# Optimization experiments

Measured on AMD Instinct MI355X. Metric: run time of the kernel, lower is better.

The kernel has to match this reference:

```python
import jax, jax.numpy as jnp
import numpy as np

EMBED_DIM = 768
HEADS = 8
HEAD_DIM = 128  # gnn_hidden_dim
OUT_DIM = HEADS * HEAD_DIM  # 1024, concat=True
NEG_SLOPE = 0.2  # PyG GATConv leaky_relu slope


def setup_inputs() -> dict:
    key = jax.random.key(0)
    ks = jax.random.split(key, 12)
    N, E = 10000, 160000
    x = jax.random.normal(ks[0], (N, EMBED_DIM), dtype=jnp.float32)
    edge_index = jax.random.randint(ks[1], (2, E), 0, N, dtype=jnp.int32)
    edge_attr = jax.random.uniform(ks[2], (E, 1), dtype=jnp.float32)
    # GATConv params (single layer, edge_dim=1)
    sc = 1.0 / np.sqrt(EMBED_DIM)
    W = jax.random.normal(ks[3], (EMBED_DIM, OUT_DIM), dtype=jnp.float32) * sc
    att_src = jax.random.normal(ks[4], (HEADS, HEAD_DIM), dtype=jnp.float32) * 0.1
    att_dst = jax.random.normal(ks[5], (HEADS, HEAD_DIM), dtype=jnp.float32) * 0.1
    W_edge = jax.random.normal(ks[6], (1, OUT_DIM), dtype=jnp.float32)
    att_edge = jax.random.normal(ks[7], (HEADS, HEAD_DIM), dtype=jnp.float32) * 0.1
    bias = jnp.zeros((OUT_DIM,), dtype=jnp.float32)
    # final classifier: in = 3*OUT_DIM (global pool + text node + image node)
    clf_W = jax.random.normal(ks[8], (3 * OUT_DIM, 2), dtype=jnp.float32) * (1.0 / np.sqrt(3 * OUT_DIM))
    clf_b = jnp.zeros((2,), dtype=jnp.float32)
    return {
        'x': x, 'edge_index': edge_index, 'edge_attr': edge_attr,
        'text_idx': 0, 'image_idx': 1,
        'W': W, 'att_src': att_src, 'att_dst': att_dst,
        'W_edge': W_edge, 'att_edge': att_edge, 'bias': bias,
        'clf_W': clf_W, 'clf_b': clf_b,
    }


def gat_layer(x, edge_index, edge_attr, W, att_src, att_dst, W_edge, att_edge, bias):
    N = x.shape[0]
    # add self-loops with edge_attr = mean of existing edge_attr (PyG default fill_value='mean')
    loop = jnp.arange(N, dtype=edge_index.dtype)
    ei = jnp.concatenate([edge_index, jnp.stack([loop, loop])], axis=1)
    ea_mean = jnp.mean(edge_attr, axis=0, keepdims=True)
    ea = jnp.concatenate([edge_attr, jnp.broadcast_to(ea_mean, (N, edge_attr.shape[1]))], axis=0)
    src, dst = ei[0], ei[1]
    xs = (x @ W).reshape(N, HEADS, HEAD_DIM)             # [N, H, C]
    a_src = jnp.einsum('nhc,hc->nh', xs, att_src)        # per-node src logits
    a_dst = jnp.einsum('nhc,hc->nh', xs, att_dst)
    e_emb = (ea @ W_edge).reshape(-1, HEADS, HEAD_DIM)   # [Etot, H, C]
    a_edge = jnp.einsum('ehc,hc->eh', e_emb, att_edge)
    alpha = jax.nn.leaky_relu(a_src[src] + a_dst[dst] + a_edge, NEG_SLOPE)  # [Etot, H]
    # softmax over incoming edges of each dst node
    m = jax.ops.segment_max(alpha, dst, num_segments=N)
    ex = jnp.exp(alpha - m[dst])
    denom = jax.ops.segment_sum(ex, dst, num_segments=N)
    w = ex / denom[dst]                                  # normalized attention [Etot, H]
    msg = xs[src] * w[:, :, None]                        # [Etot, H, C]
    out = jax.ops.segment_sum(msg, dst, num_segments=N)  # [N, H, C]
    return out.reshape(N, OUT_DIM) + bias


def reference(x, edge_index, edge_attr, text_idx, image_idx,
              W, att_src, att_dst, W_edge, att_edge, bias, clf_W, clf_b):
    # single GAT layer (num_gat_layers=1 -> no ELU/dropout after, eval mode)
    h = gat_layer(x, edge_index, edge_attr, W, att_src, att_dst, W_edge, att_edge, bias)
    g = jnp.mean(h, axis=0, keepdims=True)               # global_mean_pool, batch=None
    t = h[text_idx][None, :]
    im = h[image_idx][None, :]
    fused = jnp.concatenate([g, t, im], axis=1)          # [1, 3*OUT_DIM]
    logits = fused @ clf_W + clf_b                       # [1, 2]
    return logits
```

## Files before the change

kernel.cpp:

```cpp
#include <hip/hip_runtime.h>

#define NN 10000
#define EE 160000
#define ETOT (EE + NN)
#define EMB 768
#define ODIM 1024
#define NEG 0.2f
#define CAP 56

#define OFF_P      0
#define OFF_Q      12288
#define OFF_EAACC  12296
#define OFF_CNTD   12304
#define OFF_CNTS   22304
#define ZERO_START 12296
#define ZERO_CNT   20008
#define OFF_A      32304
#define OFF_APART  192304
#define OFF_SRCD   1472304
#define OFF_DSTS   2032304
#define OFF_PACK   2592304
#define OFF_EXD    2762304
#define OFF_EXS    7242304
#define OFF_RDEN   11722304
#define OFF_S      11802304
#define OFF_Z      11882304
#define OFF_YPART  11894592
#define OFF_FPART  12859200

__global__ __launch_bounds__(256) void k1f(
    const float* __restrict__ W, const float* __restrict__ att_src,
    const float* __restrict__ att_dst, const float* __restrict__ W_edge,
    const float* __restrict__ att_edge, const float* __restrict__ edge_attr,
    const int* __restrict__ ei, float* __restrict__ ws) {
  int b = blockIdx.x;
  if (b < 48) {
    int tid = b * 256 + threadIdx.x;
    int k = tid >> 4, j = tid & 15, h = j & 7;
    const float* att = (j < 8) ? att_src : att_dst;
    const float* wp = W + k * ODIM + h * 128;
    const float* ap = att + h * 128;
    float acc = 0.f;
    #pragma unroll 8
    for (int c = 0; c < 128; ++c) acc += wp[c] * ap[c];
    ws[OFF_P + k * 16 + j] = acc;
  } else if (b == 48) {
    if (threadIdx.x < 8) {
      int h = threadIdx.x;
      float acc = 0.f;
      #pragma unroll 8
      for (int c = 0; c < 128; ++c) acc += W_edge[h * 128 + c] * att_edge[h * 128 + c];
      ws[OFF_Q + h] = acc;
    }
  } else if (b < 113) {
    int bi = b - 49;
    float acc = 0.f;
    for (int i = bi * 256 + threadIdx.x; i < EE; i += 64 * 256) acc += edge_attr[i];
    #pragma unroll
    for (int off = 32; off > 0; off >>= 1) acc += __shfl_down(acc, off, 64);
    if ((threadIdx.x & 63) == 0) atomicAdd(&ws[OFF_EAACC], acc);
  } else {
    int e = (b - 113) * 256 + threadIdx.x;
    if (e >= ETOT) return;
    int src, dst;
    if (e < EE) { src = ei[e]; dst = ei[EE + e]; } else { src = dst = e - EE; }
    int* cntd = (int*)(ws + OFF_CNTD);
    int* cnts = (int*)(ws + OFF_CNTS);
    int pd = atomicAdd(&cntd[dst], 1);
    if (pd < CAP) ((int*)(ws + OFF_SRCD))[dst * CAP + pd] = src;
    int ps = atomicAdd(&cnts[src], 1);
    if (ps < CAP) ((int*)(ws + OFF_DSTS))[src * CAP + ps] = dst;
    ((int*)(ws + OFF_PACK))[e] = (pd & 0xffff) | (ps << 16);
  }
}

__global__ __launch_bounds__(256) void k3_part(const float* __restrict__ x,
                                               float* __restrict__ ws) {
  __shared__ float pL[96 * 16];
  const int c = blockIdx.y;
  const int kbase = c * 96;
  for (int i = threadIdx.x; i < 96 * 16; i += 256) pL[i] = ws[OFF_P + kbase * 16 + i];
  __syncthreads();
  int n = blockIdx.x * 256 + threadIdx.x;
  if (n >= NN) return;
  float acc[16];
  #pragma unroll
  for (int j = 0; j < 16; ++j) acc[j] = 0.f;
  const float4* xr = (const float4*)(x + n * EMB + kbase);
  for (int kk = 0; kk < 24; ++kk) {
    float4 xv = xr[kk];
    const float* pr = &pL[kk * 64];
    #pragma unroll
    for (int j = 0; j < 16; ++j) acc[j] += xv.x * pr[j];
    #pragma unroll
    for (int j = 0; j < 16; ++j) acc[j] += xv.y * pr[16 + j];
    #pragma unroll
    for (int j = 0; j < 16; ++j) acc[j] += xv.z * pr[32 + j];
    #pragma unroll
    for (int j = 0; j < 16; ++j) acc[j] += xv.w * pr[48 + j];
  }
  float4* ap = (float4*)(ws + OFF_APART + c * 160000 + n * 16);
  ap[0] = make_float4(acc[0], acc[1], acc[2], acc[3]);
  ap[1] = make_float4(acc[4], acc[5], acc[6], acc[7]);
  ap[2] = make_float4(acc[8], acc[9], acc[10], acc[11]);
  ap[3] = make_float4(acc[12], acc[13], acc[14], acc[15]);
}

__global__ __launch_bounds__(256) void k_reduceA(float* __restrict__ ws) {
  int i = blockIdx.x * 256 + threadIdx.x;
  if (i >= 40000) return;
  float4 r = make_float4(0.f, 0.f, 0.f, 0.f);
  #pragma unroll
  for (int c = 0; c < 8; ++c) {
    float4 a = ((const float4*)(ws + OFF_APART + c * 160000))[i];
    r.x += a.x; r.y += a.y; r.z += a.z; r.w += a.w;
  }
  ((float4*)(ws + OFF_A))[i] = r;
}

__global__ __launch_bounds__(256) void kE(const int* __restrict__ ei,
                                          const float* __restrict__ edge_attr,
                                          float* __restrict__ ws) {
  int e = blockIdx.x * 256 + threadIdx.x;
  if (e >= ETOT) return;
  int src, dst; float ea;
  if (e < EE) { src = ei[e]; dst = ei[EE + e]; ea = edge_attr[e]; }
  else { src = dst = e - EE; ea = ws[OFF_EAACC] * (1.0f / EE); }
  int pk = ((const int*)(ws + OFF_PACK))[e];
  int pd = pk & 0xffff, ps = pk >> 16;
  const float4* as4 = (const float4*)(ws + OFF_A + src * 16);
  const float4* ad4 = (const float4*)(ws + OFF_A + dst * 16 + 8);
  float4 s0 = as4[0], s1 = as4[1], d0 = ad4[0], d1 = ad4[1];
  float asrc[8] = {s0.x, s0.y, s0.z, s0.w, s1.x, s1.y, s1.z, s1.w};
  float adst[8] = {d0.x, d0.y, d0.z, d0.w, d1.x, d1.y, d1.z, d1.w};
  float ex[8];
  #pragma unroll
  for (int h = 0; h < 8; ++h) {
    float v = asrc[h] + adst[h] + ea * ws[OFF_Q + h];
    v = (v >= 0.f) ? v : NEG * v;
    ex[h] = __expf(v);
  }
  float4 e0 = make_float4(ex[0], ex[1], ex[2], ex[3]);
  float4 e1 = make_float4(ex[4], ex[5], ex[6], ex[7]);
  if (pd < CAP) {
    float4* p = (float4*)(ws + OFF_EXD + (dst * CAP + pd) * 8);
    p[0] = e0; p[1] = e1;
  }
  if (ps < CAP) {
    float4* p = (float4*)(ws + OFF_EXS + (src * CAP + ps) * 8);
    p[0] = e0; p[1] = e1;
  }
}

__global__ __launch_bounds__(256) void kD(float* __restrict__ ws) {
  int t = blockIdx.x * 256 + threadIdx.x;
  if (t >= NN * 8) return;
  int dst = t >> 3, h = t & 7;
  int deg = ((const int*)(ws + OFF_CNTD))[dst];
  if (deg > CAP) deg = CAP;
  const float* base = ws + OFF_EXD + dst * (CAP * 8) + h;
  float den = 0.f;
  for (int j = 0; j < deg; ++j) den += base[j * 8];
  ws[OFF_RDEN + dst * 8 + h] = 1.0f / den;
}

__global__ __launch_bounds__(256) void kSZ(const float* __restrict__ x,
                                           const int* __restrict__ tptr,
                                           const int* __restrict__ iptr,
                                           float* __restrict__ ws) {
  if (blockIdx.x < 313) {
    int t = blockIdx.x * 256 + threadIdx.x;
    if (t >= NN * 8) return;
    int src = t >> 3, h = t & 7;
    int deg = ((const int*)(ws + OFF_CNTS))[src];
    if (deg > CAP) deg = CAP;
    const int* dstrow = (const int*)(ws + OFF_DSTS) + src * CAP;
    const float* exrow = ws + OFF_EXS + src * (CAP * 8) + h;
    float s = 0.f;
    for (int j = 0; j < deg; ++j)
      s += exrow[j * 8] * ws[OFF_RDEN + dstrow[j] * 8 + h];
    ws[OFF_S + src * 8 + h] = s;
  } else {
    __shared__ float wL[CAP * 8];
    __shared__ int srcS[CAP];
    __shared__ int degS;
    int r = blockIdx.x - 313;
    int d = r / 3, ky = r % 3;
    int target = (d == 0) ? tptr[0] : iptr[0];
    if (threadIdx.x == 0) {
      int dg = ((const int*)(ws + OFF_CNTD))[target];
      degS = (dg > CAP) ? CAP : dg;
    }
    __syncthreads();
    int deg = degS;
    for (int idx = threadIdx.x; idx < deg * 8; idx += 256) {
      int j = idx >> 3, h = idx & 7;
      wL[idx] = ws[OFF_EXD + (target * CAP + j) * 8 + h]
              * ws[OFF_RDEN + target * 8 + h];
      if (h == 0) srcS[j] = ((const int*)(ws + OFF_SRCD))[target * CAP + j];
    }
    __syncthreads();
    int col = ky * 256 + threadIdx.x;
    float acc[8];
    #pragma unroll
    for (int h = 0; h < 8; ++h) acc[h] = 0.f;
    for (int j = 0; j < deg; ++j) {
      float xv = x[srcS[j] * EMB + col];
      const float* wv = &wL[j * 8];
      #pragma unroll
      for (int h = 0; h < 8; ++h) acc[h] += wv[h] * xv;
    }
    #pragma unroll
    for (int h = 0; h < 8; ++h) ws[OFF_Z + (d * 8 + h) * EMB + col] = acc[h];
  }
}

__global__ __launch_bounds__(256) void k7s(const float* __restrict__ x,
                                           float* __restrict__ ws) {
  __shared__ float sL[64 * 8];
  int base = blockIdx.x * 64;
  int c = blockIdx.y;
  for (int i = threadIdx.x; i < 512; i += 256) {
    int n = base + (i >> 3);
    sL[i] = (n < NN) ? ws[OFF_S + base * 8 + i] : 0.f;
  }
  __syncthreads();
  int col = c * 256 + threadIdx.x;
  float acc[8];
  #pragma unroll
  for (int h = 0; h < 8; ++h) acc[h] = 0.f;
  int nmax = (NN - base < 64) ? (NN - base) : 64;
  for (int i = 0; i < nmax; ++i) {
    float xv = x[(base + i) * EMB + col];
    const float* sv = &sL[i * 8];
    #pragma unroll
    for (int h = 0; h < 8; ++h) acc[h] += xv * sv[h];
  }
  float* yp = ws + OFF_YPART + (blockIdx.x * 3 + c) * 2048;
  #pragma unroll
  for (int h = 0; h < 8; ++h) yp[h * 256 + threadIdx.x] = acc[h];
}

__global__ __launch_bounds__(128) void k8_part(const float* __restrict__ W,
                                               float* __restrict__ ws) {
  __shared__ float vL[3 * 96];
  int h = blockIdx.x, kc = blockIdx.y;
  int kbase = kc * 96;
  for (int k = threadIdx.x; k < 96; k += 128) {
    int col = kbase + k, cc = col >> 8, ck = col & 255;
    float acc = 0.f;
    for (int b = 0; b < 157; ++b)
      acc += ws[OFF_YPART + (b * 3 + cc) * 2048 + h * 256 + ck];
    vL[k] = acc * (1.0f / NN);
  }
  for (int i = threadIdx.x; i < 192; i += 128) {
    int d = i / 96, k = i - d * 96;
    vL[96 + i] = ws[OFF_Z + (d * 8 + h) * EMB + kbase + k];
  }
  __syncthreads();
  int c = threadIdx.x;
  float a0 = 0.f, a1 = 0.f, a2 = 0.f;
  #pragma unroll 4
  for (int k = 0; k < 96; ++k) {
    float wv = W[(kbase + k) * ODIM + h * 128 + c];
    a0 += vL[k] * wv;
    a1 += vL[96 + k] * wv;
    a2 += vL[192 + k] * wv;
  }
  float* fp = ws + OFF_FPART + kc * 3072 + h * 128 + c;
  fp[0] = a0; fp[1024] = a1; fp[2048] = a2;
}

__global__ __launch_bounds__(256) void k9_logits(const float* __restrict__ clf_W,
                                                 const float* __restrict__ clf_b,
                                                 const float* __restrict__ bias,
                                                 const float* __restrict__ ws,
                                                 float* __restrict__ out) {
  float a0 = 0.f, a1 = 0.f;
  for (int i = threadIdx.x; i < 3072; i += 256) {
    float f = bias[i & 1023];
    #pragma unroll
    for (int kc = 0; kc < 8; ++kc) f += ws[OFF_FPART + kc * 3072 + i];
    a0 += f * clf_W[i * 2 + 0];
    a1 += f * clf_W[i * 2 + 1];
  }
  #pragma unroll
  for (int off = 32; off > 0; off >>= 1) {
    a0 += __shfl_down(a0, off, 64);
    a1 += __shfl_down(a1, off, 64);
  }
  __shared__ float r0[4], r1[4];
  int wid = threadIdx.x >> 6, lane = threadIdx.x & 63;
  if (lane == 0) { r0[wid] = a0; r1[wid] = a1; }
  __syncthreads();
  if (threadIdx.x == 0) {
    out[0] = r0[0] + r0[1] + r0[2] + r0[3] + clf_b[0];
    out[1] = r1[0] + r1[1] + r1[2] + r1[3] + clf_b[1];
  }
}

extern "C" void kernel_launch(void* const* d_in, const int* in_sizes, int n_in,
                              void* d_out, int out_size, void* d_ws, size_t ws_size,
                              hipStream_t stream) {
  const float* x        = (const float*)d_in[0];
  const int*   ei       = (const int*)d_in[1];
  const float* edge_attr= (const float*)d_in[2];
  const int*   tptr     = (const int*)d_in[3];
  const int*   iptr     = (const int*)d_in[4];
  const float* W        = (const float*)d_in[5];
  const float* att_src  = (const float*)d_in[6];
  const float* att_dst  = (const float*)d_in[7];
  const float* W_edge   = (const float*)d_in[8];
  const float* att_edge = (const float*)d_in[9];
  const float* bias     = (const float*)d_in[10];
  const float* clf_W    = (const float*)d_in[11];
  const float* clf_b    = (const float*)d_in[12];
  float* ws  = (float*)d_ws;
  float* out = (float*)d_out;

  hipMemsetAsync(ws + ZERO_START, 0, ZERO_CNT * sizeof(float), stream);
  k1f<<<778, 256, 0, stream>>>(W, att_src, att_dst, W_edge, att_edge, edge_attr, ei, ws);
  dim3 g3(40, 8);
  k3_part<<<g3, 256, 0, stream>>>(x, ws);
  k_reduceA<<<157, 256, 0, stream>>>(ws);
  kE<<<665, 256, 0, stream>>>(ei, edge_attr, ws);
  kD<<<313, 256, 0, stream>>>(ws);
  kSZ<<<319, 256, 0, stream>>>(x, tptr, iptr, ws);
  dim3 g7(157, 3);
  k7s<<<g7, 256, 0, stream>>>(x, ws);
  dim3 g8(8, 8);
  k8_part<<<g8, 128, 0, stream>>>(W, ws);
  k9_logits<<<1, 256, 0, stream>>>(clf_W, clf_b, bias, ws, out);
}
```

Baseline: 200.2 us.

## Fuse GAT pipeline into one cooperative persistent kernel with grid syncs

Replaces the memset plus ten-kernel chain with a single cooperative kernel that runs each stage as a grid-strided work loop separated by grid.sync(). The attention-logit projection now does the full K reduction per node, which removes the partial buffer and its separate reduce pass. Node sums are fused with the x-weighted column sums, and the final projection writes logits directly with atomics onto a bias-initialised output. The aim is to remove launch gaps and intermediate traffic, at the cost of grid-sync overhead and a grid capped at 512 blocks. The old multi-kernel path stays as a fallback when cooperative launch is unavailable.

```diff
diff --git a/kernel.cpp b/kernel.cpp
--- a/kernel.cpp
+++ b/kernel.cpp
@@ -1,4 +1,7 @@
 #include <hip/hip_runtime.h>
+#include <hip/hip_cooperative_groups.h>
+
+namespace cg = cooperative_groups;
 
 #define NN 10000
 #define EE 160000
@@ -7,28 +10,331 @@
 #define ODIM 1024
 #define NEG 0.2f
 #define CAP 56
+#define TPB 256
 
 #define OFF_P      0
 #define OFF_Q      12288
-#define OFF_EAACC  12296
-#define OFF_CNTD   12304
-#define OFF_CNTS   22304
-#define ZERO_START 12296
-#define ZERO_CNT   20008
-#define OFF_A      32304
-#define OFF_APART  192304
-#define OFF_SRCD   1472304
-#define OFF_DSTS   2032304
-#define OFF_PACK   2592304
-#define OFF_EXD    2762304
-#define OFF_EXS    7242304
-#define OFF_RDEN   11722304
-#define OFF_S      11802304
-#define OFF_Z      11882304
-#define OFF_YPART  11894592
-#define OFF_FPART  12859200
-
-__global__ __launch_bounds__(256) void k1f(
+#define OFF_EAP    12296
+#define OFF_EAACC  12552
+#define OFF_CNTD   12556
+#define OFF_CNTS   22556
+#define OFF_A      32556
+#define OFF_SRCD   192556
+#define OFF_DSTS   752556
+#define OFF_PACK   1312556
+#define OFF_EXD    1482556
+#define OFF_EXS    5962556
+#define OFF_RDEN   10442556
+#define OFF_Z      10522556
+#define OFF_YPART  10534844
+
+__global__ __launch_bounds__(TPB, 2) void mega(
+    const float* __restrict__ x, const int* __restrict__ ei,
+    const float* __restrict__ edge_attr, const int* __restrict__ tptr,
+    const int* __restrict__ iptr, const float* __restrict__ W,
+    const float* __restrict__ att_src, const float* __restrict__ att_dst,
+    const float* __restrict__ W_edge, const float* __restrict__ att_edge,
+    const float* __restrict__ bias, const float* __restrict__ clf_W,
+    const float* __restrict__ clf_b, float* __restrict__ ws,
+    float* __restrict__ out) {
+  __shared__ float smem[6144];
+  cg::grid_group grid = cg::this_grid();
+  const int t = threadIdx.x, bid = blockIdx.x;
+  const int GS = gridDim.x;
+  int* wsI = (int*)ws;
+
+  for (int i = bid * TPB + t; i < 20000; i += GS * TPB) wsI[OFF_CNTD + i] = 0;
+  for (int u = bid; u < 113; u += GS) {
+    if (u < 48) {
+      int tid = u * TPB + t, k = tid >> 4, j = tid & 15, h = j & 7;
+      const float* att = (j < 8) ? att_src : att_dst;
+      const float* wp = W + k * ODIM + h * 128;
+      const float* ap = att + h * 128;
+      float acc = 0.f;
+      #pragma unroll 8
+      for (int c = 0; c < 128; ++c) acc += wp[c] * ap[c];
+      ws[OFF_P + k * 16 + j] = acc;
+    } else if (u == 48) {
+      if (t < 8) {
+        float acc = 0.f;
+        #pragma unroll 8
+        for (int c = 0; c < 128; ++c) acc += W_edge[t * 128 + c] * att_edge[t * 128 + c];
+        ws[OFF_Q + t] = acc;
+      }
+    } else {
+      int ue = u - 49;
+      float acc = 0.f;
+      for (int i = ue * TPB + t; i < EE; i += 64 * TPB) acc += edge_attr[i];
+      #pragma unroll
+      for (int o = 32; o > 0; o >>= 1) acc += __shfl_down(acc, o, 64);
+      if ((t & 63) == 0) ws[OFF_EAP + ue * 4 + (t >> 6)] = acc;
+    }
+  }
+  grid.sync();
+
+  for (int u = bid; u < 980; u += GS) {
+    if (u < 313) {
+      int n = u * 32 + (t & 31);
+      int jp = (t >> 5) * 2;
+      float a0 = 0.f, a1 = 0.f;
+      const float4* xr = (const float4*)(x + n * EMB);
+      for (int half = 0; half < 2; ++half) {
+        __syncthreads();
+        for (int i = t; i < 1536; i += TPB)
+          ((float4*)smem)[i] = ((const float4*)(ws + OFF_P + half * 6144))[i];
+        __syncthreads();
+        if (n < NN) {
+          for (int kk = 0; kk < 96; ++kk) {
+            float4 xv = xr[half * 96 + kk];
+            int k4 = kk * 64 + jp;
+            float2 p0 = *(const float2*)&smem[k4];
+            float2 p1 = *(const float2*)&smem[k4 + 16];
+            float2 p2 = *(const float2*)&smem[k4 + 32];
+            float2 p3 = *(const float2*)&smem[k4 + 48];
+            a0 += xv.x * p0.x + xv.y * p1.x + xv.z * p2.x + xv.w * p3.x;
+            a1 += xv.x * p0.y + xv.y * p1.y + xv.z * p2.y + xv.w * p3.y;
+          }
+        }
+      }
+      if (n < NN) {
+        ws[OFF_A + n * 16 + jp] = a0;
+        ws[OFF_A + n * 16 + jp + 1] = a1;
+      }
+    } else if (u < 978) {
+      int e = (u - 313) * TPB + t;
+      if (e < ETOT) {
+        int src, dst;
+        if (e < EE) { src = ei[e]; dst = ei[EE + e]; } else { src = dst = e - EE; }
+        int pd = atomicAdd(&wsI[OFF_CNTD + dst], 1);
+        if (pd < CAP) wsI[OFF_SRCD + dst * CAP + pd] = src;
+        int ps = atomicAdd(&wsI[OFF_CNTS + src], 1);
+        if (ps < CAP) wsI[OFF_DSTS + src * CAP + ps] = dst;
+        if (pd > CAP) pd = CAP;
+        if (ps > CAP) ps = CAP;
+        wsI[OFF_PACK + e] = pd | (ps << 16);
+      }
+    } else if (u == 978) {
+      float a = 0.f;
+      if (t < 64)
+        a = ws[OFF_EAP + t] + ws[OFF_EAP + t + 64] + ws[OFF_EAP + t + 128]
+          + ws[OFF_EAP + t + 192];
+      #pragma unroll
+      for (int o = 32; o > 0; o >>= 1) a += __shfl_down(a, o, 64);
+      if (t == 0) ws[OFF_EAACC] = a;
+    }
+  }
+  grid.sync();
+
+  for (int u = bid; u < 666; u += GS) {
+    if (u < 665) {
+      int e = u * TPB + t;
+      if (e < ETOT) {
+        int src, dst; float ea;
+        if (e < EE) { src = ei[e]; dst = ei[EE + e]; ea = edge_attr[e]; }
+        else { src = dst = e - EE; ea = ws[OFF_EAACC] * (1.0f / EE); }
+        int pk = wsI[OFF_PACK + e];
+        int pd = pk & 0xffff, ps = pk >> 16;
+        const float4* as4 = (const float4*)(ws + OFF_A + src * 16);
+        const float4* ad4 = (const float4*)(ws + OFF_A + dst * 16 + 8);
+        float4 s0 = as4[0], s1 = as4[1], d0 = ad4[0], d1 = ad4[1];
+        float asr[8] = {s0.x, s0.y, s0.z, s0.w, s1.x, s1.y, s1.z, s1.w};
+        float ads[8] = {d0.x, d0.y, d0.z, d0.w, d1.x, d1.y, d1.z, d1.w};
+        float ex[8];
+        #pragma unroll
+        for (int h = 0; h < 8; ++h) {
+          float v = asr[h] + ads[h] + ea * ws[OFF_Q + h];
+          v = (v >= 0.f) ? v : NEG * v;
+          ex[h] = __expf(v);
+        }
+        float4 e0 = make_float4(ex[0], ex[1], ex[2], ex[3]);
+        float4 e1 = make_float4(ex[4], ex[5], ex[6], ex[7]);
+        if (pd < CAP) {
+          float4* p = (float4*)(ws + OFF_EXD + (dst * CAP + pd) * 8);
+          p[0] = e0; p[1] = e1;
+        }
+        if (ps < CAP) {
+          float4* p = (float4*)(ws + OFF_EXS + (src * CAP + ps) * 8);
+          p[0] = e0; p[1] = e1;
+        }
+      }
+    } else {
+      float b0 = 0.f, b1 = 0.f;
+      for (int i = t; i < 3072; i += TPB) {
+        float f = bias[i & 1023];
+        b0 += f * clf_W[2 * i];
+        b1 += f * clf_W[2 * i + 1];
+      }
+      #pragma unroll
+      for (int o = 32; o > 0; o >>= 1) {
+        b0 += __shfl_down(b0, o, 64);
+        b1 += __shfl_down(b1, o, 64);
+      }
+      __syncthreads();
+      if ((t & 63) == 0) { smem[t >> 6] = b0; smem[4 + (t >> 6)] = b1; }
+      __syncthreads();
+      if (t == 0) {
+        out[0] = clf_b[0] + smem[0] + smem[1] + smem[2] + smem[3];
+        out[1] = clf_b[1] + smem[4] + smem[5] + smem[6] + smem[7];
+      }
+    }
+  }
+  grid.sync();
+
+  for (int u = bid; u < 313; u += GS) {
+    int tg = u * TPB + t;
+    if (tg < 80000) {
+      int dst = tg >> 3, h = tg & 7;
+      int deg = wsI[OFF_CNTD + dst]; if (deg > CAP) deg = CAP;
+      const float* bp = ws + OFF_EXD + dst * (CAP * 8) + h;
+      float den = 0.f;
+      for (int j = 0; j < deg; ++j) den += bp[j * 8];
+      ws[OFF_RDEN + tg] = 1.0f / den;
+    }
+  }
+  grid.sync();
+
+  for (int u = bid; u < 163; u += GS) {
+    if (u < 157) {
+      int base = u * 64;
+      for (int w = t; w < 512; w += TPB) {
+        int n = base + (w >> 3), h = w & 7;
+        float s = 0.f;
+        if (n < NN) {
+          int deg = wsI[OFF_CNTS + n]; if (deg > CAP) deg = CAP;
+          const float* er = ws + OFF_EXS + n * (CAP * 8) + h;
+          const int* dr = wsI + OFF_DSTS + n * CAP;
+          for (int j = 0; j < deg; ++j)
+            s += er[j * 8] * ws[OFF_RDEN + dr[j] * 8 + h];
+        }
+        smem[w] = s;
+      }
+      __syncthreads();
+      int nmax = NN - base; if (nmax > 64) nmax = 64;
+      float acc[24];
+      #pragma unroll
+      for (int q = 0; q < 24; ++q) acc[q] = 0.f;
+      for (int i = 0; i < nmax; ++i) {
+        const float* xr = x + (base + i) * EMB;
+        float x0 = xr[t], x1 = xr[t + 256], x2 = xr[t + 512];
+        const float* sv = &smem[i * 8];
+        #pragma unroll
+        for (int h = 0; h < 8; ++h) {
+          acc[h] += x0 * sv[h];
+          acc[8 + h] += x1 * sv[h];
+          acc[16 + h] += x2 * sv[h];
+        }
+      }
+      float* yp = ws + OFF_YPART + u * 6144;
+      #pragma unroll
+      for (int h = 0; h < 8; ++h) {
+        yp[h * 768 + t] = acc[h];
+        yp[h * 768 + 256 + t] = acc[8 + h];
+        yp[h * 768 + 512 + t] = acc[16 + h];
+      }
+      __syncthreads();
+    } else {
+      int r = u - 157, d = r / 3, ky = r % 3;
+      int target = (d == 0) ? tptr[0] : iptr[0];
+      float* wL = smem;
+      int* srcS = (int*)(smem + 448);
+      int* degP = (int*)(smem + 508);
+      if (t == 0) { int dg = wsI[OFF_CNTD + target]; degP[0] = (dg > CAP) ? CAP : dg; }
+      __syncthreads();
+      int deg = degP[0];
+      for (int idx = t; idx < deg * 8; idx += TPB) {
+        int j = idx >> 3, h = idx & 7;
+        wL[idx] = ws[OFF_EXD + (target * CAP + j) * 8 + h] * ws[OFF_RDEN + target * 8 + h];
+        if (h == 0) srcS[j] = wsI[OFF_SRCD + target * CAP + j];
+      }
+      __syncthreads();
+      int col = ky * 256 + t;
+      float acc[8];
+      #pragma unroll
+      for (int h = 0; h < 8; ++h) acc[h] = 0.f;
+      for (int j = 0; j < deg; ++j) {
+        float xv = x[srcS[j] * EMB + col];
+        const float* wv = &wL[j * 8];
+        #pragma unroll
+        for (int h = 0; h < 8; ++h) acc[h] += wv[h] * xv;
+      }
+      #pragma unroll
+      for (int h = 0; h < 8; ++h) ws[OFF_Z + (d * 8 + h) * EMB + col] = acc[h];
+      __syncthreads();
+    }
+  }
+  grid.sync();
+
+  for (int u = bid; u < 64; u += GS) {
+    int h = u >> 3, kc = u & 7, kbase = kc * 96;
+    float* vY2 = smem;
+    float* vL  = smem + 192;
+    if (t < 192) {
+      int k = t % 96, half = t / 96;
+      float a = 0.f;
+      for (int b = half; b < 157; b += 2)
+        a += ws[OFF_YPART + b * 6144 + h * 768 + kbase + k];
+      vY2[t] = a;
+    } else {
+      for (int i = t - 192; i < 192; i += 64) {
+        int d = i / 96, k = i - d * 96;
+        vL[96 + i] = ws[OFF_Z + (d * 8 + h) * EMB + kbase + k];
+      }
+    }
+    __syncthreads();
+    if (t < 96) vL[t] = (vY2[t] + vY2[t + 96]) * (1.0f / NN);
+    __syncthreads();
+    float l0 = 0.f, l1 = 0.f;
+    if (t < 128) {
+      int c = t;
+      float a0 = 0.f, a1 = 0.f, a2 = 0.f;
+      #pragma unroll 4
+      for (int k = 0; k < 96; ++k) {
+        float wv = W[(kbase + k) * ODIM + h * 128 + c];
+        a0 += vL[k] * wv;
+        a1 += vL[96 + k] * wv;
+        a2 += vL[192 + k] * wv;
+      }
+      int ib = h * 128 + c;
+      l0 = a0 * clf_W[2 * ib] + a1 * clf_W[2 * (1024 + ib)] + a2 * clf_W[2 * (2048 + ib)];
+      l1 = a0 * clf_W[2 * ib + 1] + a1 * clf_W[2 * (1024 + ib) + 1] + a2 * clf_W[2 * (2048 + ib) + 1];
+    }
+    #pragma unroll
+    for (int o = 32; o > 0; o >>= 1) {
+      l0 += __shfl_down(l0, o, 64);
+      l1 += __shfl_down(l1, o, 64);
+    }
+    __syncthreads();
+    if ((t & 63) == 0) { smem[480 + (t >> 6)] = l0; smem[484 + (t >> 6)] = l1; }
+    __syncthreads();
+    if (t == 0) {
+      atomicAdd(&out[0], smem[480] + smem[481] + smem[482] + smem[483]);
+      atomicAdd(&out[1], smem[484] + smem[485] + smem[486] + smem[487]);
+    }
+    __syncthreads();
+  }
+}
+
+#define FB_P      0
+#define FB_Q      12288
+#define FB_EAACC  12296
+#define FB_CNTD   12304
+#define FB_CNTS   22304
+#define FB_ZSTART 12296
+#define FB_ZCNT   20008
+#define FB_A      32304
+#define FB_APART  192304
+#define FB_SRCD   1472304
+#define FB_DSTS   2032304
+#define FB_PACK   2592304
+#define FB_EXD    2762304
+#define FB_EXS    7242304
+#define FB_RDEN   11722304
+#define FB_S      11802304
+#define FB_Z      11882304
+#define FB_YPART  11894592
+#define FB_FPART  12859200
+
+__global__ __launch_bounds__(256) void f_k1f(
     const float* __restrict__ W, const float* __restrict__ att_src,
     const float* __restrict__ att_dst, const float* __restrict__ W_edge,
     const float* __restrict__ att_edge, const float* __restrict__ edge_attr,
@@ -43,14 +349,14 @@
     float acc = 0.f;
     #pragma unroll 8
     for (int c = 0; c < 128; ++c) acc += wp[c] * ap[c];
-    ws[OFF_P + k * 16 + j] = acc;
+    ws[FB_P + k * 16 + j] = acc;
   } else if (b == 48) {
     if (threadIdx.x < 8) {
       int h = threadIdx.x;
       float acc = 0.f;
       #pragma unroll 8
       for (int c = 0; c < 128; ++c) acc += W_edge[h * 128 + c] * att_edge[h * 128 + c];
-      ws[OFF_Q + h] = acc;
+      ws[FB_Q + h] = acc;
     }
   } else if (b < 113) {
     int bi = b - 49;
@@ -58,28 +364,30 @@
     for (int i = bi * 256 + threadIdx.x; i < EE; i += 64 * 256) acc += edge_attr[i];
     #pragma unroll
     for (int off = 32; off > 0; off >>= 1) acc += __shfl_down(acc, off, 64);
-    if ((threadIdx.x & 63) == 0) atomicAdd(&ws[OFF_EAACC], acc);
+    if ((threadIdx.x & 63) == 0) atomicAdd(&ws[FB_EAACC], acc);
   } else {
     int e = (b - 113) * 256 + threadIdx.x;
     if (e >= ETOT) return;
     int src, dst;
     if (e < EE) { src = ei[e]; dst = ei[EE + e]; } else { src = dst = e - EE; }
-    int* cntd = (int*)(ws + OFF_CNTD);
-    int* cnts = (int*)(ws + OFF_CNTS);
+    int* cntd = (int*)(ws + FB_CNTD);
+    int* cnts = (int*)(ws + FB_CNTS);
     int pd = atomicAdd(&cntd[dst], 1);
-    if (pd < CAP) ((int*)(ws + OFF_SRCD))[dst * CAP + pd] = src;
+    if (pd < CAP) ((int*)(ws + FB_SRCD))[dst * CAP + pd] = src;
     int ps = atomicAdd(&cnts[src], 1);
-    if (ps < CAP) ((int*)(ws + OFF_DSTS))[src * CAP + ps] = dst;
-    ((int*)(ws + OFF_PACK))[e] = (pd & 0xffff) | (ps << 16);
-  }
-}
-
-__global__ __launch_bounds__(256) void k3_part(const float* __restrict__ x,
-                                               float* __restrict__ ws) {
+    if (ps < CAP) ((int*)(ws + FB_DSTS))[src * CAP + ps] = dst;
+    if (pd > CAP) pd = CAP;
+    if (ps > CAP) ps = CAP;
+    ((int*)(ws + FB_PACK))[e] = pd | (ps << 16);
+  }
+}
+
+__global__ __launch_bounds__(256) void f_k3part(const float* __restrict__ x,
+                                                float* __restrict__ ws) {
   __shared__ float pL[96 * 16];
   const int c = blockIdx.y;
   const int kbase = c * 96;
-  for (int i = threadIdx.x; i < 96 * 16; i += 256) pL[i] = ws[OFF_P + kbase * 16 + i];
+  for (int i = threadIdx.x; i < 96 * 16; i += 256) pL[i] = ws[FB_P + kbase * 16 + i];
   __syncthreads();
   int n = blockIdx.x * 256 + threadIdx.x;
   if (n >= NN) return;
@@ -99,87 +407,87 @@
     #pragma unroll
     for (int j = 0; j < 16; ++j) acc[j] += xv.w * pr[48 + j];
   }
-  float4* ap = (float4*)(ws + OFF_APART + c * 160000 + n * 16);
+  float4* ap = (float4*)(ws + FB_APART + c * 160000 + n * 16);
   ap[0] = make_float4(acc[0], acc[1], acc[2], acc[3]);
   ap[1] = make_float4(acc[4], acc[5], acc[6], acc[7]);
   ap[2] = make_float4(acc[8], acc[9], acc[10], acc[11]);
   ap[3] = make_float4(acc[12], acc[13], acc[14], acc[15]);
 }
 
-__global__ __launch_bounds__(256) void k_reduceA(float* __restrict__ ws) {
+__global__ __launch_bounds__(256) void f_reduceA(float* __restrict__ ws) {
   int i = blockIdx.x * 256 + threadIdx.x;
   if (i >= 40000) return;
   float4 r = make_float4(0.f, 0.f, 0.f, 0.f);
   #pragma unroll
   for (int c = 0; c < 8; ++c) {
-    float4 a = ((const float4*)(ws + OFF_APART + c * 160000))[i];
+    float4 a = ((const float4*)(ws + FB_APART + c * 160000))[i];
     r.x += a.x; r.y += a.y; r.z += a.z; r.w += a.w;
   }
-  ((float4*)(ws + OFF_A))[i] = r;
-}
-
-__global__ __launch_bounds__(256) void kE(const int* __restrict__ ei,
-                                          const float* __restrict__ edge_attr,
-                                          float* __restrict__ ws) {
+  ((float4*)(ws + FB_A))[i] = r;
+}
+
+__global__ __launch_bounds__(256) void f_kE(const int* __restrict__ ei,
+                                            const float* __restrict__ edge_attr,
+                                            float* __restrict__ ws) {
   int e = blockIdx.x * 256 + threadIdx.x;
   if (e >= ETOT) return;
   int src, dst; float ea;
   if (e < EE) { src = ei[e]; dst = ei[EE + e]; ea = edge_attr[e]; }
-  else { src = dst = e - EE; ea = ws[OFF_EAACC] * (1.0f / EE); }
-  int pk = ((const int*)(ws + OFF_PACK))[e];
+  else { src = dst = e - EE; ea = ws[FB_EAACC] * (1.0f / EE); }
+  int pk = ((const int*)(ws + FB_PACK))[e];
   int pd = pk & 0xffff, ps = pk >> 16;
-  const float4* as4 = (const float4*)(ws + OFF_A + src * 16);
-  const float4* ad4 = (const float4*)(ws + OFF_A + dst * 16 + 8);
+  const float4* as4 = (const float4*)(ws + FB_A + src * 16);
+  const float4* ad4 = (const float4*)(ws + FB_A + dst * 16 + 8);
   float4 s0 = as4[0], s1 = as4[1], d0 = ad4[0], d1 = ad4[1];
-  float asrc[8] = {s0.x, s0.y, s0.z, s0.w, s1.x, s1.y, s1.z, s1.w};
-  float adst[8] = {d0.x, d0.y, d0.z, d0.w, d1.x, d1.y, d1.z, d1.w};
+  float asr[8] = {s0.x, s0.y, s0.z, s0.w, s1.x, s1.y, s1.z, s1.w};
+  float ads[8] = {d0.x, d0.y, d0.z, d0.w, d1.x, d1.y, d1.z, d1.w};
   float ex[8];
   #pragma unroll
   for (int h = 0; h < 8; ++h) {
-    float v = asrc[h] + adst[h] + ea * ws[OFF_Q + h];
+    float v = asr[h] + ads[h] + ea * ws[FB_Q + h];
     v = (v >= 0.f) ? v : NEG * v;
     ex[h] = __expf(v);
   }
   float4 e0 = make_float4(ex[0], ex[1], ex[2], ex[3]);
   float4 e1 = make_float4(ex[4], ex[5], ex[6], ex[7]);
   if (pd < CAP) {
-    float4* p = (float4*)(ws + OFF_EXD + (dst * CAP + pd) * 8);
+    float4* p = (float4*)(ws + FB_EXD + (dst * CAP + pd) * 8);
     p[0] = e0; p[1] = e1;
   }
   if (ps < CAP) {
-    float4* p = (float4*)(ws + OFF_EXS + (src * CAP + ps) * 8);
+    float4* p = (float4*)(ws + FB_EXS + (src * CAP + ps) * 8);
     p[0] = e0; p[1] = e1;
   }
 }
 
-__global__ __launch_bounds__(256) void kD(float* __restrict__ ws) {
+__global__ __launch_bounds__(256) void f_kD(float* __restrict__ ws) {
   int t = blockIdx.x * 256 + threadIdx.x;
   if (t >= NN * 8) return;
   int dst = t >> 3, h = t & 7;
-  int deg = ((const int*)(ws + OFF_CNTD))[dst];
+  int deg = ((const int*)(ws + FB_CNTD))[dst];
   if (deg > CAP) deg = CAP;
-  const float* base = ws + OFF_EXD + dst * (CAP * 8) + h;
+  const float* base = ws + FB_EXD + dst * (CAP * 8) + h;
   float den = 0.f;
   for (int j = 0; j < deg; ++j) den += base[j * 8];
-  ws[OFF_RDEN + dst * 8 + h] = 1.0f / den;
-}
-
-__global__ __launch_bounds__(256) void kSZ(const float* __restrict__ x,
-                                           const int* __restrict__ tptr,
-                                           const int* __restrict__ iptr,
-                                           float* __restrict__ ws) {
+  ws[FB_RDEN + dst * 8 + h] = 1.0f / den;
+}
+
+__global__ __launch_bounds__(256) void f_kSZ(const float* __restrict__ x,
+                                             const int* __restrict__ tptr,
+                                             const int* __restrict__ iptr,
+                                             float* __restrict__ ws) {
   if (blockIdx.x < 313) {
     int t = blockIdx.x * 256 + threadIdx.x;
     if (t >= NN * 8) return;
     int src = t >> 3, h = t & 7;
-    int deg = ((const int*)(ws + OFF_CNTS))[src];
+    int deg = ((const int*)(ws + FB_CNTS))[src];
     if (deg > CAP) deg = CAP;
-    const int* dstrow = (const int*)(ws + OFF_DSTS) + src * CAP;
-    const float* exrow = ws + OFF_EXS + src * (CAP * 8) + h;
+    const int* dstrow = (const int*)(ws + FB_DSTS) + src * CAP;
+    const float* exrow = ws + FB_EXS + src * (CAP * 8) + h;
     float s = 0.f;
     for (int j = 0; j < deg; ++j)
-      s += exrow[j * 8] * ws[OFF_RDEN + dstrow[j] * 8 + h];
-    ws[OFF_S + src * 8 + h] = s;
+      s += exrow[j * 8] * ws[FB_RDEN + dstrow[j] * 8 + h];
+    ws[FB_S + src * 8 + h] = s;
   } else {
     __shared__ float wL[CAP * 8];
     __shared__ int srcS[CAP];
@@ -188,16 +496,15 @@
     int d = r / 3, ky = r % 3;
     int target = (d == 0) ? tptr[0] : iptr[0];
     if (threadIdx.x == 0) {
-      int dg = ((const int*)(ws + OFF_CNTD))[target];
+      int dg = ((const int*)(ws + FB_CNTD))[target];
       degS = (dg > CAP) ? CAP : dg;
     }
     __syncthreads();
     int deg = degS;
     for (int idx = threadIdx.x; idx < deg * 8; idx += 256) {
       int j = idx >> 3, h = idx & 7;
-      wL[idx] = ws[OFF_EXD + (target * CAP + j) * 8 + h]
-              * ws[OFF_RDEN + target * 8 + h];
-      if (h == 0) srcS[j] = ((const int*)(ws + OFF_SRCD))[target * CAP + j];
+      wL[idx] = ws[FB_EXD + (target * CAP + j) * 8 + h] * ws[FB_RDEN + target * 8 + h];
+      if (h == 0) srcS[j] = ((const int*)(ws + FB_SRCD))[target * CAP + j];
     }
     __syncthreads();
     int col = ky * 256 + threadIdx.x;
@@ -211,18 +518,18 @@
       for (int h = 0; h < 8; ++h) acc[h] += wv[h] * xv;
     }
     #pragma unroll
-    for (int h = 0; h < 8; ++h) ws[OFF_Z + (d * 8 + h) * EMB + col] = acc[h];
-  }
-}
-
-__global__ __launch_bounds__(256) void k7s(const float* __restrict__ x,
-                                           float* __restrict__ ws) {
+    for (int h = 0; h < 8; ++h) ws[FB_Z + (d * 8 + h) * EMB + col] = acc[h];
+  }
+}
+
+__global__ __launch_bounds__(256) void f_k7s(const float* __restrict__ x,
+                                             float* __restrict__ ws) {
   __shared__ float sL[64 * 8];
   int base = blockIdx.x * 64;
   int c = blockIdx.y;
   for (int i = threadIdx.x; i < 512; i += 256) {
     int n = base + (i >> 3);
-    sL[i] = (n < NN) ? ws[OFF_S + base * 8 + i] : 0.f;
+    sL[i] = (n < NN) ? ws[FB_S + base * 8 + i] : 0.f;
   }
   __syncthreads();
   int col = c * 256 + threadIdx.x;
@@ -236,13 +543,13 @@
     #pragma unroll
     for (int h = 0; h < 8; ++h) acc[h] += xv * sv[h];
   }
-  float* yp = ws + OFF_YPART + (blockIdx.x * 3 + c) * 2048;
+  float* yp = ws + FB_YPART + (blockIdx.x * 3 + c) * 2048;
   #pragma unroll
   for (int h = 0; h < 8; ++h) yp[h * 256 + threadIdx.x] = acc[h];
 }
 
-__global__ __launch_bounds__(128) void k8_part(const float* __restrict__ W,
-                                               float* __restrict__ ws) {
+__global__ __launch_bounds__(128) void f_k8part(const float* __restrict__ W,
+                                                float* __restrict__ ws) {
   __shared__ float vL[3 * 96];
   int h = blockIdx.x, kc = blockIdx.y;
   int kbase = kc * 96;
@@ -250,12 +557,12 @@
     int col = kbase + k, cc = col >> 8, ck = col & 255;
     float acc = 0.f;
     for (int b = 0; b < 157; ++b)
-      acc += ws[OFF_YPART + (b * 3 + cc) * 2048 + h * 256 + ck];
+      acc += ws[FB_YPART + (b * 3 + cc) * 2048 + h * 256 + ck];
     vL[k] = acc * (1.0f / NN);
   }
   for (int i = threadIdx.x; i < 192; i += 128) {
     int d = i / 96, k = i - d * 96;
-    vL[96 + i] = ws[OFF_Z + (d * 8 + h) * EMB + kbase + k];
+    vL[96 + i] = ws[FB_Z + (d * 8 + h) * EMB + kbase + k];
   }
   __syncthreads();
   int c = threadIdx.x;
@@ -267,20 +574,20 @@
     a1 += vL[96 + k] * wv;
     a2 += vL[192 + k] * wv;
   }
-  float* fp = ws + OFF_FPART + kc * 3072 + h * 128 + c;
+  float* fp = ws + FB_FPART + kc * 3072 + h * 128 + c;
   fp[0] = a0; fp[1024] = a1; fp[2048] = a2;
 }
 
-__global__ __launch_bounds__(256) void k9_logits(const float* __restrict__ clf_W,
-                                                 const float* __restrict__ clf_b,
-                                                 const float* __restrict__ bias,
-                                                 const float* __restrict__ ws,
-                                                 float* __restrict__ out) {
+__global__ __launch_bounds__(256) void f_k9(const float* __restrict__ clf_W,
+                                            const float* __restrict__ clf_b,
+                                            const float* __restrict__ bias,
+                                            const float* __restrict__ ws,
+                                            float* __restrict__ out) {
   float a0 = 0.f, a1 = 0.f;
   for (int i = threadIdx.x; i < 3072; i += 256) {
     float f = bias[i & 1023];
     #pragma unroll
-    for (int kc = 0; kc < 8; ++kc) f += ws[OFF_FPART + kc * 3072 + i];
+    for (int kc = 0; kc < 8; ++kc) f += ws[FB_FPART + kc * 3072 + i];
     a0 += f * clf_W[i * 2 + 0];
     a1 += f * clf_W[i * 2 + 1];
   }
@@ -318,17 +625,41 @@
   float* ws  = (float*)d_ws;
   float* out = (float*)d_out;
 
-  hipMemsetAsync(ws + ZERO_START, 0, ZERO_CNT * sizeof(float), stream);
-  k1f<<<778, 256, 0, stream>>>(W, att_src, att_dst, W_edge, att_edge, edge_attr, ei, ws);
-  dim3 g3(40, 8);
-  k3_part<<<g3, 256, 0, stream>>>(x, ws);
-  k_reduceA<<<157, 256, 0, stream>>>(ws);
-  kE<<<665, 256, 0, stream>>>(ei, edge_attr, ws);
-  kD<<<313, 256, 0, stream>>>(ws);
-  kSZ<<<319, 256, 0, stream>>>(x, tptr, iptr, ws);
-  dim3 g7(157, 3);
-  k7s<<<g7, 256, 0, stream>>>(x, ws);
-  dim3 g8(8, 8);
-  k8_part<<<g8, 128, 0, stream>>>(W, ws);
-  k9_logits<<<1, 256, 0, stream>>>(clf_W, clf_b, bias, ws, out);
-}
+  int dev = 0, coop = 0, cus = 0, maxb = 0;
+  hipGetDevice(&dev);
+  hipDeviceGetAttribute(&coop, hipDeviceAttributeCooperativeLaunch, dev);
+  hipDeviceGetAttribute(&cus, hipDeviceAttributeMultiprocessorCount, dev);
+  hipOccupancyMaxActiveBlocksPerMultiprocessor(&maxb, mega, TPB, 0);
+  long maxgrid = (long)maxb * (long)cus;
+  int grid = (maxgrid > 512) ? 512 : (int)maxgrid;
+
+  bool launched = false;
+  if (coop && grid >= 8) {
+    void* kargs[] = {
+      (void*)&x, (void*)&ei, (void*)&edge_attr, (void*)&tptr, (void*)&iptr,
+      (void*)&W, (void*)&att_src, (void*)&att_dst, (void*)&W_edge,
+      (void*)&att_edge, (void*)&bias, (void*)&clf_W, (void*)&clf_b,
+      (void*)&ws, (void*)&out
+    };
+    hipError_t err = hipLaunchCooperativeKernel((void*)mega, dim3(grid), dim3(TPB),
+                                                kargs, 0, stream);
+    launched = (err == hipSuccess);
+  }
+
+  if (!launched) {
+    hipMemsetAsync(ws + FB_ZSTART, 0, FB_ZCNT * sizeof(float), stream);
+    f_k1f<<<778, 256, 0, stream>>>(W, att_src, att_dst, W_edge, att_edge,
+                                   edge_attr, ei, ws);
+    dim3 g3(40, 8);
+    f_k3part<<<g3, 256, 0, stream>>>(x, ws);
+    f_reduceA<<<157, 256, 0, stream>>>(ws);
+    f_kE<<<665, 256, 0, stream>>>(ei, edge_attr, ws);
+    f_kD<<<313, 256, 0, stream>>>(ws);
+    f_kSZ<<<319, 256, 0, stream>>>(x, tptr, iptr, ws);
+    dim3 g7(157, 3);
+    f_k7s<<<g7, 256, 0, stream>>>(x, ws);
+    dim3 g8(8, 8);
+    f_k8part<<<g8, 128, 0, stream>>>(W, ws);
+    f_k9<<<1, 256, 0, stream>>>(clf_W, clf_b, bias, ws, out);
+  }
+}
```

After: 522.1 us. 161% more time.
